# Kernel tuning notes

Measured on AMD Instinct MI355X. Metric: run time of the kernel, lower is better.

## Reference

```python
import jax, jax.numpy as jnp
import numpy as np

B = 1024          # batch
N = 2048          # number of gene groups
G = 32            # uniform group size (sum of gene_groups = N*G = 65536)
H1 = 2048         # hidden1_size
H2 = 512          # hidden2_size
EPS = 1e-5        # BatchNorm eps
SLOPE = 0.05      # LeakyReLU negative slope


def lrelu(v):
    return jnp.where(v >= 0, v, SLOPE * v)


def setup_inputs() -> dict:
    key = jax.random.key(0)
    ks = jax.random.split(key, 12)
    x = jax.random.normal(ks[0], (B, N * G), dtype=jnp.float32)
    # per-group Linear(G, 1) weights, stacked: [N, G] weights + [N] biases
    Wg = jax.random.normal(ks[1], (N, G), dtype=jnp.float32) / np.sqrt(G)
    bg = jax.random.normal(ks[2], (N,), dtype=jnp.float32) * 0.01
    att_w = jax.random.normal(ks[3], (N,), dtype=jnp.float32)
    W1 = jax.random.normal(ks[4], (N, H1), dtype=jnp.float32) / np.sqrt(N)
    b1 = jnp.zeros((H1,), dtype=jnp.float32)
    W2 = jax.random.normal(ks[5], (H1, H2), dtype=jnp.float32) / np.sqrt(H1)
    b2 = jnp.zeros((H2,), dtype=jnp.float32)
    Wo = jax.random.normal(ks[6], (H2, 1), dtype=jnp.float32) / np.sqrt(H2)
    bo = jnp.zeros((1,), dtype=jnp.float32)
    gamma1 = jnp.ones((H1,), dtype=jnp.float32)
    beta1 = jnp.zeros((H1,), dtype=jnp.float32)
    gamma2 = jnp.ones((H2,), dtype=jnp.float32)
    beta2 = jnp.zeros((H2,), dtype=jnp.float32)
    return dict(x=x, Wg=Wg, bg=bg, att_w=att_w, W1=W1, b1=b1,
                gamma1=gamma1, beta1=beta1, W2=W2, b2=b2,
                gamma2=gamma2, beta2=beta2, Wo=Wo, bo=bo)


def batchnorm(h, gamma, beta):
    # training-mode BatchNorm1d: batch statistics, biased variance
    mu = jnp.mean(h, axis=0)
    var = jnp.mean(jnp.square(h - mu), axis=0)
    return (h - mu) * jax.lax.rsqrt(var + EPS) * gamma + beta


def reference(x, Wg, bg, att_w, W1, b1, gamma1, beta1, W2, b2, gamma2, beta2, Wo, bo):
    # fused per-group linear + LeakyReLU: x viewed as [B, N, G]
    xg = x.reshape(B, N, G)
    g = lrelu(jnp.einsum('bng,ng->bn', xg, Wg) + bg)       # [B, N]
    att = jax.nn.softmax(att_w)                             # [N]
    a = g * att                                             # [B, N]
    h1 = lrelu(batchnorm(a @ W1 + b1, gamma1, beta1))       # [B, H1]
    h2 = lrelu(batchnorm(h1 @ W2 + b2, gamma2, beta2))      # [B, H2]
    return h2 @ Wo + bo                                     # [B, 1]
```

## Files before the change

kernel.cpp:

```cpp
#include <hip/hip_runtime.h>
#include <hip/hip_bf16.h>

#define B_DIM   1024
#define N_DIM   2048
#define G_DIM   32
#define H1_DIM  2048
#define H2_DIM  512
#define BN_EPS  1e-5f
#define SLOPE   0.05f

typedef short v8s __attribute__((ext_vector_type(8)));
typedef float v4f __attribute__((ext_vector_type(4)));

__device__ __forceinline__ float lrelu_f(float v) { return v >= 0.f ? v : SLOPE * v; }
__device__ __forceinline__ float bf2f(unsigned short u) {
    union { unsigned int i; float f; } c; c.i = ((unsigned int)u) << 16; return c.f;
}
__device__ __forceinline__ unsigned short f2bf(float f) {
    __hip_bfloat16 h = __float2bfloat16(f);
    return *(unsigned short*)&h;
}

#define GLOAD_LDS16(gp, lp)                                                              \
    __builtin_amdgcn_global_load_lds(                                                    \
        (const __attribute__((address_space(1))) unsigned int*)(gp),                     \
        (__attribute__((address_space(3))) unsigned int*)(lp), 16, 0, 0)

__global__ __launch_bounds__(256) void prep_kernel(
        const float* __restrict__ x, const float* __restrict__ Wg,
        const float* __restrict__ bg, __hip_bfloat16* __restrict__ g,
        const float* __restrict__ W1, const float* __restrict__ W2,
        const float* __restrict__ aw,
        __hip_bfloat16* __restrict__ W1T, __hip_bfloat16* __restrict__ W2T) {
    __shared__ float tile[64][65];
    __shared__ float red[8];
    __shared__ float scl[64];
    int t = threadIdx.x;
    int bid = blockIdx.x;

    if (bid < 2048) {
        int brow = bid >> 4;
        int seg = bid & 15;
        int gl = t >> 1, half = t & 1;
        int n = seg * 128 + gl;
        float4 wv[4];
        const float4* wsrc = (const float4*)(Wg + (size_t)n * 32 + half * 16);
#pragma unroll
        for (int q = 0; q < 4; ++q) wv[q] = wsrc[q];
        float bgv = bg[n];
#pragma unroll
        for (int bb = 0; bb < 8; ++bb) {
            int b = brow * 8 + bb;
            const float4* xr = (const float4*)(x + (size_t)b * (N_DIM * G_DIM) +
                                               (size_t)n * 32 + half * 16);
            float s = 0.f;
#pragma unroll
            for (int q = 0; q < 4; ++q) {
                float4 v = xr[q];
                s += v.x * wv[q].x + v.y * wv[q].y + v.z * wv[q].z + v.w * wv[q].w;
            }
            s += __shfl_xor(s, 1, 64);
            if (half == 0)
                g[(size_t)b * N_DIM + n] = __float2bfloat16(lrelu_f(s + bgv));
        }
        return;
    }

    const float* W;
    __hip_bfloat16* Wt;
    int Kd, Jd, j0, k0;
    bool doScale;
    int tb = bid - 2048;
    if (tb < 1024) {
        W = W1; Wt = W1T; Kd = N_DIM; Jd = H1_DIM;
        j0 = (tb & 31) * 64; k0 = (tb >> 5) * 64; doScale = true;
        float mx = -1e30f;
#pragma unroll
        for (int i = 0; i < 8; ++i) mx = fmaxf(mx, aw[t + i * 256]);
#pragma unroll
        for (int off = 32; off; off >>= 1) mx = fmaxf(mx, __shfl_xor(mx, off, 64));
        if ((t & 63) == 0) red[t >> 6] = mx;
        __syncthreads();
        float M = fmaxf(fmaxf(red[0], red[1]), fmaxf(red[2], red[3]));
        float sm = 0.f;
#pragma unroll
        for (int i = 0; i < 8; ++i) sm += expf(aw[t + i * 256] - M);
#pragma unroll
        for (int off = 32; off; off >>= 1) sm += __shfl_xor(sm, off, 64);
        if ((t & 63) == 0) red[4 + (t >> 6)] = sm;
        __syncthreads();
        float invS = 1.f / (red[4] + red[5] + red[6] + red[7]);
        if (t < 64) scl[t] = expf(aw[k0 + t] - M) * invS;
        __syncthreads();
    } else {
        int b2 = tb - 1024;
        W = W2; Wt = W2T; Kd = H1_DIM; Jd = H2_DIM;
        j0 = (b2 & 7) * 64; k0 = (b2 >> 3) * 64; doScale = false;
    }
#pragma unroll
    for (int p = 0; p < 16; ++p) {
        int r = (t >> 6) + p * 4;
        float v = W[(size_t)(k0 + r) * Jd + j0 + (t & 63)];
        if (doScale) v *= scl[r];
        tile[r][t & 63] = v;
    }
    __syncthreads();
#pragma unroll
    for (int p = 0; p < 8; ++p) {
        int jr = (t >> 5) + p * 8;
        int kc = (t & 31) * 2;
        ushort2 pk;
        pk.x = f2bf(tile[kc][jr]);
        pk.y = f2bf(tile[kc + 1][jr]);
        *(ushort2*)(Wt + (size_t)(j0 + jr) * Kd + k0 + kc) = pk;
    }
}

__global__ __launch_bounds__(512) void gemm1_stats(
        const __hip_bfloat16* __restrict__ A, const __hip_bfloat16* __restrict__ Bt,
        __hip_bfloat16* __restrict__ C, float* __restrict__ ps, float* __restrict__ pq,
        int N, int K) {
    __shared__ __hip_bfloat16 A_s[2][64 * 64];
    __shared__ __hip_bfloat16 B_s[2][128 * 64];
    __shared__ float rs[2][128], rq[2][128];

    int bid = blockIdx.y * 16 + blockIdx.x;
    int wg  = (bid & 7) * 32 + (bid >> 3);
    int bx  = wg & 15, by = wg >> 4;

    int tid = threadIdx.x, lane = tid & 63, wave = tid >> 6;
    int wr = wave >> 2, wc = wave & 3;
    int rbase = bx * 64, cbase = by * 128;
    int l15 = lane & 15, kq = lane >> 4;

    v4f acc[2][2] = {};

    auto stage = [&](int buf, int kt) {
        int k0 = kt << 6;
        {
            int s = tid;
            int row = s >> 3, cg = (s & 7) ^ (row & 7);
            GLOAD_LDS16(A + (size_t)(rbase + row) * K + k0 + cg * 8, (char*)A_s[buf] + s * 16);
        }
#pragma unroll
        for (int i = 0; i < 2; ++i) {
            int s = tid + i * 512;
            int row = s >> 3, cg = (s & 7) ^ (row & 7);
            GLOAD_LDS16(Bt + (size_t)(cbase + row) * K + k0 + cg * 8, (char*)B_s[buf] + s * 16);
        }
    };

    const int nkt = K >> 6;
    stage(0, 0);
    __syncthreads();
    int cur = 0;
    for (int kt = 0; kt < nkt; ++kt) {
        if (kt + 1 < nkt) stage(cur ^ 1, kt + 1);
#pragma unroll
        for (int kc = 0; kc < 2; ++kc) {
            v8s af[2], bfv[2];
#pragma unroll
            for (int m = 0; m < 2; ++m) {
                int row = wr * 32 + m * 16 + l15;
                int off = row * 128 + ((((kc << 2) + kq) ^ (row & 7)) << 4);
                af[m] = *(const v8s*)((const char*)A_s[cur] + off);
            }
#pragma unroll
            for (int n = 0; n < 2; ++n) {
                int row = wc * 32 + n * 16 + l15;
                int off = row * 128 + ((((kc << 2) + kq) ^ (row & 7)) << 4);
                bfv[n] = *(const v8s*)((const char*)B_s[cur] + off);
            }
            __builtin_amdgcn_s_setprio(1);
#pragma unroll
            for (int m = 0; m < 2; ++m)
#pragma unroll
                for (int n = 0; n < 2; ++n)
                    acc[m][n] = __builtin_amdgcn_mfma_f32_16x16x32_bf16(af[m], bfv[n],
                                                                        acc[m][n], 0, 0, 0);
            __builtin_amdgcn_s_setprio(0);
        }
        __syncthreads();
        cur ^= 1;
    }

    int crow = kq * 4;
#pragma unroll
    for (int m = 0; m < 2; ++m)
#pragma unroll
        for (int n = 0; n < 2; ++n) {
            int r = rbase + wr * 32 + m * 16 + crow;
            int c = cbase + wc * 32 + n * 16 + l15;
#pragma unroll
            for (int i = 0; i < 4; ++i)
                C[(size_t)(r + i) * N + c] = __float2bfloat16(acc[m][n][i]);
        }

    float cs[2], cq[2];
#pragma unroll
    for (int n = 0; n < 2; ++n) {
        cs[n] = 0.f; cq[n] = 0.f;
#pragma unroll
        for (int m = 0; m < 2; ++m)
#pragma unroll
            for (int i = 0; i < 4; ++i) {
                float v = acc[m][n][i];
                cs[n] += v; cq[n] += v * v;
            }
#pragma unroll
        for (int off = 16; off <= 32; off <<= 1) {
            cs[n] += __shfl_xor(cs[n], off, 64);
            cq[n] += __shfl_xor(cq[n], off, 64);
        }
    }
    if (lane < 16) {
#pragma unroll
        for (int n = 0; n < 2; ++n) {
            rs[wr][wc * 32 + n * 16 + lane] = cs[n];
            rq[wr][wc * 32 + n * 16 + lane] = cq[n];
        }
    }
    __syncthreads();
    if (tid < 128) {
        ps[(size_t)bx * N + cbase + tid] = rs[0][tid] + rs[1][tid];
        pq[(size_t)bx * N + cbase + tid] = rq[0][tid] + rq[1][tid];
    }
}

template<int BN_T, int TT, typename OutT>
__global__ __launch_bounds__(TT) void gemm_stats(
        const __hip_bfloat16* __restrict__ A, const __hip_bfloat16* __restrict__ Bt,
        OutT* __restrict__ C, float* __restrict__ ps, float* __restrict__ pq,
        int N, int K) {
    constexpr int WC = BN_T / 32;
    constexpr int WR = TT / 64 / WC;
    __shared__ __hip_bfloat16 A_s[2][64 * 128];
    __shared__ __hip_bfloat16 B_s[2][BN_T * 128];
    __shared__ float rs[WR][BN_T], rq[WR][BN_T];

    int nwg = gridDim.x * gridDim.y;
    int bid = blockIdx.y * gridDim.x + blockIdx.x;
    int cpx = nwg >> 3;
    int wg  = (bid & 7) * cpx + (bid >> 3);
    int bx  = wg % gridDim.x, by = wg / gridDim.x;

    int tid = threadIdx.x, lane = tid & 63, wave = tid >> 6;
    int wr = wave / WC, wc = wave % WC;
    int rbase = bx * 64, cbase = by * BN_T;
    int l15 = lane & 15, kq = lane >> 4;

    v4f acc[2][2] = {};

    auto stage = [&](int buf, int kt) {
        int k0 = kt << 7;
#pragma unroll
        for (int i = 0; i < 1024 / TT; ++i) {
            int s = tid + i * TT;
            int row = s >> 4, cg = (s & 15) ^ (row & 15);
            GLOAD_LDS16(A + (size_t)(rbase + row) * K + k0 + cg * 8, (char*)A_s[buf] + s * 16);
        }
#pragma unroll
        for (int i = 0; i < BN_T * 16 / TT; ++i) {
            int s = tid + i * TT;
            int row = s >> 4, cg = (s & 15) ^ (row & 15);
            GLOAD_LDS16(Bt + (size_t)(cbase + row) * K + k0 + cg * 8, (char*)B_s[buf] + s * 16);
        }
    };

    const int nkt = K >> 7;
    stage(0, 0);
    __syncthreads();
    int cur = 0;
    for (int kt = 0; kt < nkt; ++kt) {
        if (kt + 1 < nkt) stage(cur ^ 1, kt + 1);
#pragma unroll
        for (int kc = 0; kc < 4; ++kc) {
            v8s af[2], bfv[2];
#pragma unroll
            for (int m = 0; m < 2; ++m) {
                int row = wr * 32 + m * 16 + l15;
                int off = row * 256 + (((kc * 4 + kq) ^ (row & 15)) << 4);
                af[m] = *(const v8s*)((const char*)A_s[cur] + off);
            }
#pragma unroll
            for (int n = 0; n < 2; ++n) {
                int row = wc * 32 + n * 16 + l15;
                int off = row * 256 + (((kc * 4 + kq) ^ (row & 15)) << 4);
                bfv[n] = *(const v8s*)((const char*)B_s[cur] + off);
            }
            __builtin_amdgcn_s_setprio(1);
#pragma unroll
            for (int m = 0; m < 2; ++m)
#pragma unroll
                for (int n = 0; n < 2; ++n)
                    acc[m][n] = __builtin_amdgcn_mfma_f32_16x16x32_bf16(af[m], bfv[n],
                                                                        acc[m][n], 0, 0, 0);
            __builtin_amdgcn_s_setprio(0);
        }
        __syncthreads();
        cur ^= 1;
    }

    int crow = kq * 4;
#pragma unroll
    for (int m = 0; m < 2; ++m)
#pragma unroll
        for (int n = 0; n < 2; ++n) {
            int r = rbase + wr * 32 + m * 16 + crow;
            int c = cbase + wc * 32 + n * 16 + l15;
#pragma unroll
            for (int i = 0; i < 4; ++i) {
                float v = acc[m][n][i];
                if constexpr (sizeof(OutT) == 2)
                    ((__hip_bfloat16*)C)[(size_t)(r + i) * N + c] = __float2bfloat16(v);
                else
                    ((float*)C)[(size_t)(r + i) * N + c] = v;
            }
        }

    float cs[2], cq[2];
#pragma unroll
    for (int n = 0; n < 2; ++n) {
        cs[n] = 0.f; cq[n] = 0.f;
#pragma unroll
        for (int m = 0; m < 2; ++m)
#pragma unroll
            for (int i = 0; i < 4; ++i) {
                float v = acc[m][n][i];
                cs[n] += v; cq[n] += v * v;
            }
#pragma unroll
        for (int off = 16; off <= 32; off <<= 1) {
            cs[n] += __shfl_xor(cs[n], off, 64);
            cq[n] += __shfl_xor(cq[n], off, 64);
        }
    }
    if (lane < 16) {
#pragma unroll
        for (int n = 0; n < 2; ++n) {
            rs[wr][wc * 32 + n * 16 + lane] = cs[n];
            rq[wr][wc * 32 + n * 16 + lane] = cq[n];
        }
    }
    __syncthreads();
    if (tid < BN_T) {
        float s = 0.f, q = 0.f;
#pragma unroll
        for (int w = 0; w < WR; ++w) { s += rs[w][tid]; q += rq[w][tid]; }
        ps[(size_t)bx * N + cbase + tid] = s;
        pq[(size_t)bx * N + cbase + tid] = q;
    }
}

__global__ __launch_bounds__(256) void bn_apply_fused(
        const __hip_bfloat16* __restrict__ hpre,
        const float* __restrict__ ps, const float* __restrict__ pq,
        const float* __restrict__ gamma, const float* __restrict__ beta,
        __hip_bfloat16* __restrict__ o) {
    __shared__ float scl[H1_DIM], shf[H1_DIM];
    int t = threadIdx.x;
#pragma unroll
    for (int p = 0; p < 8; ++p) {
        int c = t + p * 256;
        float s = 0.f, q = 0.f;
#pragma unroll
        for (int i = 0; i < 16; ++i) {
            s += ps[i * H1_DIM + c];
            q += pq[i * H1_DIM + c];
        }
        float mu = s * (1.f / B_DIM);
        float var = fmaxf(q * (1.f / B_DIM) - mu * mu, 0.f);
        float rsv = rsqrtf(var + BN_EPS);
        float sc = rsv * gamma[c];
        scl[c] = sc;
        shf[c] = beta[c] - mu * sc;
    }
    __syncthreads();
    int j = t * 8;
    float4 sc0 = *(const float4*)&scl[j];
    float4 sc1 = *(const float4*)&scl[j + 4];
    float4 sh0 = *(const float4*)&shf[j];
    float4 sh1 = *(const float4*)&shf[j + 4];
#pragma unroll
    for (int rr = 0; rr < 8; ++rr) {
        size_t base = (size_t)(blockIdx.x * 8 + rr) * H1_DIM + j;
        v8s v = *(const v8s*)(hpre + base);
        v8s pk;
        pk[0] = (short)f2bf(lrelu_f(bf2f((unsigned short)v[0]) * sc0.x + sh0.x));
        pk[1] = (short)f2bf(lrelu_f(bf2f((unsigned short)v[1]) * sc0.y + sh0.y));
        pk[2] = (short)f2bf(lrelu_f(bf2f((unsigned short)v[2]) * sc0.z + sh0.z));
        pk[3] = (short)f2bf(lrelu_f(bf2f((unsigned short)v[3]) * sc0.w + sh0.w));
        pk[4] = (short)f2bf(lrelu_f(bf2f((unsigned short)v[4]) * sc1.x + sh1.x));
        pk[5] = (short)f2bf(lrelu_f(bf2f((unsigned short)v[5]) * sc1.y + sh1.y));
        pk[6] = (short)f2bf(lrelu_f(bf2f((unsigned short)v[6]) * sc1.z + sh1.z));
        pk[7] = (short)f2bf(lrelu_f(bf2f((unsigned short)v[7]) * sc1.w + sh1.w));
        *(v8s*)(o + base) = pk;
    }
}

__global__ __launch_bounds__(256) void bn_dot_fused(
        const float* __restrict__ h2,
        const float* __restrict__ ps, const float* __restrict__ pq,
        const float* __restrict__ gamma, const float* __restrict__ beta,
        const float* __restrict__ Wo, const float* __restrict__ bo,
        float* __restrict__ out) {
    __shared__ float scl[H2_DIM], shf[H2_DIM];
    __shared__ float red[4][4];
    int t = threadIdx.x;
#pragma unroll
    for (int p = 0; p < 2; ++p) {
        int c = t + p * 256;
        float s = 0.f, q = 0.f;
#pragma unroll
        for (int i = 0; i < 16; ++i) {
            s += ps[i * H2_DIM + c];
            q += pq[i * H2_DIM + c];
        }
        float mu = s * (1.f / B_DIM);
        float var = fmaxf(q * (1.f / B_DIM) - mu * mu, 0.f);
        float rsv = rsqrtf(var + BN_EPS);
        float sc = rsv * gamma[c];
        scl[c] = sc;
        shf[c] = beta[c] - mu * sc;
    }
    __syncthreads();
    float accv[4];
#pragma unroll
    for (int r = 0; r < 4; ++r) {
        int b = blockIdx.x * 4 + r;
        float s = 0.f;
#pragma unroll
        for (int p = 0; p < 2; ++p) {
            int jj = t + p * 256;
            float v = lrelu_f(h2[(size_t)b * H2_DIM + jj] * scl[jj] + shf[jj]);
            s += v * Wo[jj];
        }
#pragma unroll
        for (int off = 32; off; off >>= 1) s += __shfl_down(s, off, 64);
        accv[r] = s;
    }
    if ((t & 63) == 0) {
#pragma unroll
        for (int r = 0; r < 4; ++r) red[t >> 6][r] = accv[r];
    }
    __syncthreads();
    if (t < 4)
        out[blockIdx.x * 4 + t] = red[0][t] + red[1][t] + red[2][t] + red[3][t] + bo[0];
}

extern "C" void kernel_launch(void* const* d_in, const int* in_sizes, int n_in,
                              void* d_out, int out_size, void* d_ws, size_t ws_size,
                              hipStream_t stream) {
    const float* x     = (const float*)d_in[0];
    const float* Wg    = (const float*)d_in[1];
    const float* bg    = (const float*)d_in[2];
    const float* att_w = (const float*)d_in[3];
    const float* W1    = (const float*)d_in[4];
    const float* gamma1 = (const float*)d_in[6];
    const float* beta1  = (const float*)d_in[7];
    const float* W2    = (const float*)d_in[8];
    const float* gamma2 = (const float*)d_in[10];
    const float* beta2  = (const float*)d_in[11];
    const float* Wo    = (const float*)d_in[12];
    const float* bo    = (const float*)d_in[13];
    float* out = (float*)d_out;

    char* ws = (char*)d_ws;
    size_t off = 0;
    auto alloc = [&](size_t bytes) {
        void* p = ws + off;
        off = (off + bytes + 255) & ~(size_t)255;
        return p;
    };
    __hip_bfloat16* W1T    = (__hip_bfloat16*)alloc((size_t)H1_DIM * N_DIM * 2);
    __hip_bfloat16* W2T    = (__hip_bfloat16*)alloc((size_t)H2_DIM * H1_DIM * 2);
    __hip_bfloat16* g      = (__hip_bfloat16*)alloc((size_t)B_DIM * N_DIM * 2);
    __hip_bfloat16* h1pre  = (__hip_bfloat16*)alloc((size_t)B_DIM * H1_DIM * 2);
    __hip_bfloat16* h1     = (__hip_bfloat16*)alloc((size_t)B_DIM * H1_DIM * 2);
    float*          h2raw  = (float*)alloc((size_t)B_DIM * H2_DIM * 4);
    float*          ps     = (float*)alloc(16 * H1_DIM * 4);
    float*          pq     = (float*)alloc(16 * H1_DIM * 4);
    (void)ws_size; (void)in_sizes; (void)n_in; (void)out_size;

    prep_kernel<<<dim3(2048 + 1024 + 256), 256, 0, stream>>>(x, Wg, bg, g,
                                                             W1, W2, att_w, W1T, W2T);
    gemm1_stats<<<dim3(16, 16), 512, 0, stream>>>(g, W1T, h1pre, ps, pq, H1_DIM, N_DIM);
    bn_apply_fused<<<dim3(B_DIM / 8), 256, 0, stream>>>(h1pre, ps, pq, gamma1, beta1, h1);
    gemm_stats<32, 128, float><<<dim3(B_DIM / 64, H2_DIM / 32), 128, 0, stream>>>(
        h1, W2T, h2raw, ps, pq, H2_DIM, H1_DIM);
    bn_dot_fused<<<dim3(B_DIM / 4), 256, 0, stream>>>(h2raw, ps, pq, gamma2, beta2, Wo, bo, out);
}
```

Before: 114.7 us.

## Fuse BN1 apply into GEMM2 A-staging and retile GEMM1 to 64x64

```diff
diff --git a/kernel.cpp b/kernel.cpp
--- a/kernel.cpp
+++ b/kernel.cpp
@@ -116,137 +116,20 @@
     }
 }
 
-__global__ __launch_bounds__(512) void gemm1_stats(
+__global__ __launch_bounds__(256) void gemm1_stats(
         const __hip_bfloat16* __restrict__ A, const __hip_bfloat16* __restrict__ Bt,
-        __hip_bfloat16* __restrict__ C, float* __restrict__ ps, float* __restrict__ pq,
-        int N, int K) {
-    __shared__ __hip_bfloat16 A_s[2][64 * 64];
-    __shared__ __hip_bfloat16 B_s[2][128 * 64];
-    __shared__ float rs[2][128], rq[2][128];
-
-    int bid = blockIdx.y * 16 + blockIdx.x;
-    int wg  = (bid & 7) * 32 + (bid >> 3);
+        __hip_bfloat16* __restrict__ C, float* __restrict__ ps, float* __restrict__ pq) {
+    __shared__ __hip_bfloat16 A_s[2][64 * 128];
+    __shared__ __hip_bfloat16 B_s[2][64 * 128];
+    __shared__ float rs[2][64], rq[2][64];
+
+    int bid = blockIdx.x;
+    int wg  = (bid & 7) * 64 + (bid >> 3);
     int bx  = wg & 15, by = wg >> 4;
 
     int tid = threadIdx.x, lane = tid & 63, wave = tid >> 6;
-    int wr = wave >> 2, wc = wave & 3;
-    int rbase = bx * 64, cbase = by * 128;
-    int l15 = lane & 15, kq = lane >> 4;
-
-    v4f acc[2][2] = {};
-
-    auto stage = [&](int buf, int kt) {
-        int k0 = kt << 6;
-        {
-            int s = tid;
-            int row = s >> 3, cg = (s & 7) ^ (row & 7);
-            GLOAD_LDS16(A + (size_t)(rbase + row) * K + k0 + cg * 8, (char*)A_s[buf] + s * 16);
-        }
-#pragma unroll
-        for (int i = 0; i < 2; ++i) {
-            int s = tid + i * 512;
-            int row = s >> 3, cg = (s & 7) ^ (row & 7);
-            GLOAD_LDS16(Bt + (size_t)(cbase + row) * K + k0 + cg * 8, (char*)B_s[buf] + s * 16);
-        }
-    };
-
-    const int nkt = K >> 6;
-    stage(0, 0);
-    __syncthreads();
-    int cur = 0;
-    for (int kt = 0; kt < nkt; ++kt) {
-        if (kt + 1 < nkt) stage(cur ^ 1, kt + 1);
-#pragma unroll
-        for (int kc = 0; kc < 2; ++kc) {
-            v8s af[2], bfv[2];
-#pragma unroll
-            for (int m = 0; m < 2; ++m) {
-                int row = wr * 32 + m * 16 + l15;
-                int off = row * 128 + ((((kc << 2) + kq) ^ (row & 7)) << 4);
-                af[m] = *(const v8s*)((const char*)A_s[cur] + off);
-            }
-#pragma unroll
-            for (int n = 0; n < 2; ++n) {
-                int row = wc * 32 + n * 16 + l15;
-                int off = row * 128 + ((((kc << 2) + kq) ^ (row & 7)) << 4);
-                bfv[n] = *(const v8s*)((const char*)B_s[cur] + off);
-            }
-            __builtin_amdgcn_s_setprio(1);
-#pragma unroll
-            for (int m = 0; m < 2; ++m)
-#pragma unroll
-                for (int n = 0; n < 2; ++n)
-                    acc[m][n] = __builtin_amdgcn_mfma_f32_16x16x32_bf16(af[m], bfv[n],
-                                                                        acc[m][n], 0, 0, 0);
-            __builtin_amdgcn_s_setprio(0);
-        }
-        __syncthreads();
-        cur ^= 1;
-    }
-
-    int crow = kq * 4;
-#pragma unroll
-    for (int m = 0; m < 2; ++m)
-#pragma unroll
-        for (int n = 0; n < 2; ++n) {
-            int r = rbase + wr * 32 + m * 16 + crow;
-            int c = cbase + wc * 32 + n * 16 + l15;
-#pragma unroll
-            for (int i = 0; i < 4; ++i)
-                C[(size_t)(r + i) * N + c] = __float2bfloat16(acc[m][n][i]);
-        }
-
-    float cs[2], cq[2];
-#pragma unroll
-    for (int n = 0; n < 2; ++n) {
-        cs[n] = 0.f; cq[n] = 0.f;
-#pragma unroll
-        for (int m = 0; m < 2; ++m)
-#pragma unroll
-            for (int i = 0; i < 4; ++i) {
-                float v = acc[m][n][i];
-                cs[n] += v; cq[n] += v * v;
-            }
-#pragma unroll
-        for (int off = 16; off <= 32; off <<= 1) {
-            cs[n] += __shfl_xor(cs[n], off, 64);
-            cq[n] += __shfl_xor(cq[n], off, 64);
-        }
-    }
-    if (lane < 16) {
-#pragma unroll
-        for (int n = 0; n < 2; ++n) {
-            rs[wr][wc * 32 + n * 16 + lane] = cs[n];
-            rq[wr][wc * 32 + n * 16 + lane] = cq[n];
-        }
-    }
-    __syncthreads();
-    if (tid < 128) {
-        ps[(size_t)bx * N + cbase + tid] = rs[0][tid] + rs[1][tid];
-        pq[(size_t)bx * N + cbase + tid] = rq[0][tid] + rq[1][tid];
-    }
-}
-
-template<int BN_T, int TT, typename OutT>
-__global__ __launch_bounds__(TT) void gemm_stats(
-        const __hip_bfloat16* __restrict__ A, const __hip_bfloat16* __restrict__ Bt,
-        OutT* __restrict__ C, float* __restrict__ ps, float* __restrict__ pq,
-        int N, int K) {
-    constexpr int WC = BN_T / 32;
-    constexpr int WR = TT / 64 / WC;
-    __shared__ __hip_bfloat16 A_s[2][64 * 128];
-    __shared__ __hip_bfloat16 B_s[2][BN_T * 128];
-    __shared__ float rs[WR][BN_T], rq[WR][BN_T];
-
-    int nwg = gridDim.x * gridDim.y;
-    int bid = blockIdx.y * gridDim.x + blockIdx.x;
-    int cpx = nwg >> 3;
-    int wg  = (bid & 7) * cpx + (bid >> 3);
-    int bx  = wg % gridDim.x, by = wg / gridDim.x;
-
-    int tid = threadIdx.x, lane = tid & 63, wave = tid >> 6;
-    int wr = wave / WC, wc = wave % WC;
-    int rbase = bx * 64, cbase = by * BN_T;
+    int wr = wave >> 1, wc = wave & 1;
+    int rbase = bx * 64, cbase = by * 64;
     int l15 = lane & 15, kq = lane >> 4;
 
     v4f acc[2][2] = {};
@@ -254,25 +137,26 @@
     auto stage = [&](int buf, int kt) {
         int k0 = kt << 7;
 #pragma unroll
-        for (int i = 0; i < 1024 / TT; ++i) {
-            int s = tid + i * TT;
+        for (int i = 0; i < 4; ++i) {
+            int s = tid + i * 256;
             int row = s >> 4, cg = (s & 15) ^ (row & 15);
-            GLOAD_LDS16(A + (size_t)(rbase + row) * K + k0 + cg * 8, (char*)A_s[buf] + s * 16);
-        }
-#pragma unroll
-        for (int i = 0; i < BN_T * 16 / TT; ++i) {
-            int s = tid + i * TT;
+            GLOAD_LDS16(A + (size_t)(rbase + row) * N_DIM + k0 + cg * 8,
+                        (char*)A_s[buf] + s * 16);
+        }
+#pragma unroll
+        for (int i = 0; i < 4; ++i) {
+            int s = tid + i * 256;
             int row = s >> 4, cg = (s & 15) ^ (row & 15);
-            GLOAD_LDS16(Bt + (size_t)(cbase + row) * K + k0 + cg * 8, (char*)B_s[buf] + s * 16);
+            GLOAD_LDS16(Bt + (size_t)(cbase + row) * N_DIM + k0 + cg * 8,
+                        (char*)B_s[buf] + s * 16);
         }
     };
 
-    const int nkt = K >> 7;
     stage(0, 0);
     __syncthreads();
     int cur = 0;
-    for (int kt = 0; kt < nkt; ++kt) {
-        if (kt + 1 < nkt) stage(cur ^ 1, kt + 1);
+    for (int kt = 0; kt < 16; ++kt) {
+        if (kt + 1 < 16) stage(cur ^ 1, kt + 1);
 #pragma unroll
         for (int kc = 0; kc < 4; ++kc) {
             v8s af[2], bfv[2];
@@ -309,13 +193,8 @@
             int r = rbase + wr * 32 + m * 16 + crow;
             int c = cbase + wc * 32 + n * 16 + l15;
 #pragma unroll
-            for (int i = 0; i < 4; ++i) {
-                float v = acc[m][n][i];
-                if constexpr (sizeof(OutT) == 2)
-                    ((__hip_bfloat16*)C)[(size_t)(r + i) * N + c] = __float2bfloat16(v);
-                else
-                    ((float*)C)[(size_t)(r + i) * N + c] = v;
-            }
+            for (int i = 0; i < 4; ++i)
+                C[(size_t)(r + i) * H1_DIM + c] = __float2bfloat16(acc[m][n][i]);
         }
 
     float cs[2], cq[2];
@@ -343,58 +222,150 @@
         }
     }
     __syncthreads();
-    if (tid < BN_T) {
+    if (tid < 64) {
+        ps[(size_t)bx * H1_DIM + cbase + tid] = rs[0][tid] + rs[1][tid];
+        pq[(size_t)bx * H1_DIM + cbase + tid] = rq[0][tid] + rq[1][tid];
+    }
+}
+
+__global__ __launch_bounds__(256) void gemm2_bn1(
+        const __hip_bfloat16* __restrict__ h1pre, const __hip_bfloat16* __restrict__ W2T,
+        float* __restrict__ h2raw,
+        const float* __restrict__ ps1, const float* __restrict__ pq1,
+        const float* __restrict__ gamma1, const float* __restrict__ beta1,
+        float* __restrict__ ps2, float* __restrict__ pq2) {
+    __shared__ float scl[H1_DIM], shf[H1_DIM];
+    __shared__ __hip_bfloat16 A2[2][64 * 128];
+    __shared__ __hip_bfloat16 B2[2][32 * 128];
+    __shared__ float rs2[4][32], rq2[4][32];
+
+    int tid = threadIdx.x, lane = tid & 63, wave = tid >> 6;
+    int l15 = lane & 15, kq = lane >> 4;
+
+#pragma unroll
+    for (int p = 0; p < 8; ++p) {
+        int c = tid + p * 256;
         float s = 0.f, q = 0.f;
 #pragma unroll
-        for (int w = 0; w < WR; ++w) { s += rs[w][tid]; q += rq[w][tid]; }
-        ps[(size_t)bx * N + cbase + tid] = s;
-        pq[(size_t)bx * N + cbase + tid] = q;
-    }
-}
-
-__global__ __launch_bounds__(256) void bn_apply_fused(
-        const __hip_bfloat16* __restrict__ hpre,
-        const float* __restrict__ ps, const float* __restrict__ pq,
-        const float* __restrict__ gamma, const float* __restrict__ beta,
-        __hip_bfloat16* __restrict__ o) {
-    __shared__ float scl[H1_DIM], shf[H1_DIM];
-    int t = threadIdx.x;
-#pragma unroll
-    for (int p = 0; p < 8; ++p) {
-        int c = t + p * 256;
-        float s = 0.f, q = 0.f;
-#pragma unroll
         for (int i = 0; i < 16; ++i) {
-            s += ps[i * H1_DIM + c];
-            q += pq[i * H1_DIM + c];
+            s += ps1[i * H1_DIM + c];
+            q += pq1[i * H1_DIM + c];
         }
         float mu = s * (1.f / B_DIM);
         float var = fmaxf(q * (1.f / B_DIM) - mu * mu, 0.f);
         float rsv = rsqrtf(var + BN_EPS);
-        float sc = rsv * gamma[c];
+        float sc = rsv * gamma1[c];
         scl[c] = sc;
-        shf[c] = beta[c] - mu * sc;
-    }
-    __syncthreads();
-    int j = t * 8;
-    float4 sc0 = *(const float4*)&scl[j];
-    float4 sc1 = *(const float4*)&scl[j + 4];
-    float4 sh0 = *(const float4*)&shf[j];
-    float4 sh1 = *(const float4*)&shf[j + 4];
-#pragma unroll
-    for (int rr = 0; rr < 8; ++rr) {
-        size_t base = (size_t)(blockIdx.x * 8 + rr) * H1_DIM + j;
-        v8s v = *(const v8s*)(hpre + base);
-        v8s pk;
-        pk[0] = (short)f2bf(lrelu_f(bf2f((unsigned short)v[0]) * sc0.x + sh0.x));
-        pk[1] = (short)f2bf(lrelu_f(bf2f((unsigned short)v[1]) * sc0.y + sh0.y));
-        pk[2] = (short)f2bf(lrelu_f(bf2f((unsigned short)v[2]) * sc0.z + sh0.z));
-        pk[3] = (short)f2bf(lrelu_f(bf2f((unsigned short)v[3]) * sc0.w + sh0.w));
-        pk[4] = (short)f2bf(lrelu_f(bf2f((unsigned short)v[4]) * sc1.x + sh1.x));
-        pk[5] = (short)f2bf(lrelu_f(bf2f((unsigned short)v[5]) * sc1.y + sh1.y));
-        pk[6] = (short)f2bf(lrelu_f(bf2f((unsigned short)v[6]) * sc1.z + sh1.z));
-        pk[7] = (short)f2bf(lrelu_f(bf2f((unsigned short)v[7]) * sc1.w + sh1.w));
-        *(v8s*)(o + base) = pk;
+        shf[c] = beta1[c] - mu * sc;
+    }
+    __syncthreads();
+
+    int bid = blockIdx.x;
+    int wg = (bid & 7) * 32 + (bid >> 3);
+    int bxx = wg & 15, byy = wg >> 4;
+    int rb = bxx * 64, cb = byy * 32;
+
+    v4f acc2[2] = {};
+
+    auto stageA2 = [&](int buf, int kt) {
+        int k0 = kt << 7;
+#pragma unroll
+        for (int i = 0; i < 4; ++i) {
+            int s = tid + i * 256;
+            int row = s >> 4, cc = s & 15;
+            v8s hv = *(const v8s*)(h1pre + (size_t)(rb + row) * H1_DIM + k0 + cc * 8);
+            int kk = k0 + cc * 8;
+            float4 s0 = *(const float4*)&scl[kk];
+            float4 s1 = *(const float4*)&scl[kk + 4];
+            float4 f0 = *(const float4*)&shf[kk];
+            float4 f1 = *(const float4*)&shf[kk + 4];
+            v8s pk;
+            pk[0] = (short)f2bf(lrelu_f(bf2f((unsigned short)hv[0]) * s0.x + f0.x));
+            pk[1] = (short)f2bf(lrelu_f(bf2f((unsigned short)hv[1]) * s0.y + f0.y));
+            pk[2] = (short)f2bf(lrelu_f(bf2f((unsigned short)hv[2]) * s0.z + f0.z));
+            pk[3] = (short)f2bf(lrelu_f(bf2f((unsigned short)hv[3]) * s0.w + f0.w));
+            pk[4] = (short)f2bf(lrelu_f(bf2f((unsigned short)hv[4]) * s1.x + f1.x));
+            pk[5] = (short)f2bf(lrelu_f(bf2f((unsigned short)hv[5]) * s1.y + f1.y));
+            pk[6] = (short)f2bf(lrelu_f(bf2f((unsigned short)hv[6]) * s1.z + f1.z));
+            pk[7] = (short)f2bf(lrelu_f(bf2f((unsigned short)hv[7]) * s1.w + f1.w));
+            *(v8s*)((char*)A2[buf] + (row * 16 + (cc ^ (row & 15))) * 16) = pk;
+        }
+    };
+    auto stageB2 = [&](int buf, int kt) {
+        int k0 = kt << 7;
+#pragma unroll
+        for (int i = 0; i < 2; ++i) {
+            int s = tid + i * 256;
+            int row = s >> 4, cg2 = (s & 15) ^ (row & 15);
+            GLOAD_LDS16(W2T + (size_t)(cb + row) * H1_DIM + k0 + cg2 * 8,
+                        (char*)B2[buf] + s * 16);
+        }
+    };
+
+    stageB2(0, 0);
+    stageA2(0, 0);
+    __syncthreads();
+    int cur = 0;
+    for (int kt = 0; kt < 16; ++kt) {
+        if (kt + 1 < 16) { stageB2(cur ^ 1, kt + 1); stageA2(cur ^ 1, kt + 1); }
+#pragma unroll
+        for (int kc = 0; kc < 4; ++kc) {
+            int arow = wave * 16 + l15;
+            v8s af = *(const v8s*)((const char*)A2[cur] +
+                                   arow * 256 + (((kc * 4 + kq) ^ (arow & 15)) << 4));
+            v8s bf0 = *(const v8s*)((const char*)B2[cur] +
+                                    l15 * 256 + (((kc * 4 + kq) ^ (l15 & 15)) << 4));
+            int brow1 = 16 + l15;
+            v8s bf1 = *(const v8s*)((const char*)B2[cur] +
+                                    brow1 * 256 + (((kc * 4 + kq) ^ (brow1 & 15)) << 4));
+            __builtin_amdgcn_s_setprio(1);
+            acc2[0] = __builtin_amdgcn_mfma_f32_16x16x32_bf16(af, bf0, acc2[0], 0, 0, 0);
+            acc2[1] = __builtin_amdgcn_mfma_f32_16x16x32_bf16(af, bf1, acc2[1], 0, 0, 0);
+            __builtin_amdgcn_s_setprio(0);
+        }
+        __syncthreads();
+        cur ^= 1;
+    }
+
+    int crow = kq * 4;
+#pragma unroll
+    for (int n = 0; n < 2; ++n) {
+        int r = rb + wave * 16 + crow;
+        int c = cb + n * 16 + l15;
+#pragma unroll
+        for (int i = 0; i < 4; ++i)
+            h2raw[(size_t)(r + i) * H2_DIM + c] = acc2[n][i];
+    }
+
+    float cs[2], cq[2];
+#pragma unroll
+    for (int n = 0; n < 2; ++n) {
+        cs[n] = 0.f; cq[n] = 0.f;
+#pragma unroll
+        for (int i = 0; i < 4; ++i) {
+            float v = acc2[n][i];
+            cs[n] += v; cq[n] += v * v;
+        }
+#pragma unroll
+        for (int off = 16; off <= 32; off <<= 1) {
+            cs[n] += __shfl_xor(cs[n], off, 64);
+            cq[n] += __shfl_xor(cq[n], off, 64);
+        }
+    }
+    if (lane < 16) {
+#pragma unroll
+        for (int n = 0; n < 2; ++n) {
+            rs2[wave][n * 16 + lane] = cs[n];
+            rq2[wave][n * 16 + lane] = cq[n];
+        }
+    }
+    __syncthreads();
+    if (tid < 32) {
+        float s = 0.f, q = 0.f;
+#pragma unroll
+        for (int w = 0; w < 4; ++w) { s += rs2[w][tid]; q += rq2[w][tid]; }
+        ps2[(size_t)bxx * H2_DIM + cb + tid] = s;
+        pq2[(size_t)bxx * H2_DIM + cb + tid] = q;
     }
 }
 
@@ -472,21 +443,22 @@
         off = (off + bytes + 255) & ~(size_t)255;
         return p;
     };
-    __hip_bfloat16* W1T    = (__hip_bfloat16*)alloc((size_t)H1_DIM * N_DIM * 2);
-    __hip_bfloat16* W2T    = (__hip_bfloat16*)alloc((size_t)H2_DIM * H1_DIM * 2);
-    __hip_bfloat16* g      = (__hip_bfloat16*)alloc((size_t)B_DIM * N_DIM * 2);
-    __hip_bfloat16* h1pre  = (__hip_bfloat16*)alloc((size_t)B_DIM * H1_DIM * 2);
-    __hip_bfloat16* h1     = (__hip_bfloat16*)alloc((size_t)B_DIM * H1_DIM * 2);
-    float*          h2raw  = (float*)alloc((size_t)B_DIM * H2_DIM * 4);
-    float*          ps     = (float*)alloc(16 * H1_DIM * 4);
-    float*          pq     = (float*)alloc(16 * H1_DIM * 4);
+    __hip_bfloat16* W1T   = (__hip_bfloat16*)alloc((size_t)H1_DIM * N_DIM * 2);
+    __hip_bfloat16* W2T   = (__hip_bfloat16*)alloc((size_t)H2_DIM * H1_DIM * 2);
+    __hip_bfloat16* g     = (__hip_bfloat16*)alloc((size_t)B_DIM * N_DIM * 2);
+    __hip_bfloat16* h1pre = (__hip_bfloat16*)alloc((size_t)B_DIM * H1_DIM * 2);
+    float*          h2raw = (float*)alloc((size_t)B_DIM * H2_DIM * 4);
+    float*          ps1   = (float*)alloc(16 * H1_DIM * 4);
+    float*          pq1   = (float*)alloc(16 * H1_DIM * 4);
+    float*          ps2   = (float*)alloc(16 * H2_DIM * 4);
+    float*          pq2   = (float*)alloc(16 * H2_DIM * 4);
     (void)ws_size; (void)in_sizes; (void)n_in; (void)out_size;
 
     prep_kernel<<<dim3(2048 + 1024 + 256), 256, 0, stream>>>(x, Wg, bg, g,
                                                              W1, W2, att_w, W1T, W2T);
-    gemm1_stats<<<dim3(16, 16), 512, 0, stream>>>(g, W1T, h1pre, ps, pq, H1_DIM, N_DIM);
-    bn_apply_fused<<<dim3(B_DIM / 8), 256, 0, stream>>>(h1pre, ps, pq, gamma1, beta1, h1);
-    gemm_stats<32, 128, float><<<dim3(B_DIM / 64, H2_DIM / 32), 128, 0, stream>>>(
-        h1, W2T, h2raw, ps, pq, H2_DIM, H1_DIM);
-    bn_dot_fused<<<dim3(B_DIM / 4), 256, 0, stream>>>(h2raw, ps, pq, gamma2, beta2, Wo, bo, out);
-}
+    gemm1_stats<<<dim3(512), 256, 0, stream>>>(g, W1T, h1pre, ps1, pq1);
+    gemm2_bn1<<<dim3(256), 256, 0, stream>>>(h1pre, W2T, h2raw, ps1, pq1,
+                                             gamma1, beta1, ps2, pq2);
+    bn_dot_fused<<<dim3(B_DIM / 4), 256, 0, stream>>>(h2raw, ps2, pq2, gamma2, beta2,
+                                                      Wo, bo, out);
+}
```

Result: faster. 104.3 us (-9.1%).
